# Kernel optimization log

Hardware: AMD Instinct MI355X
Metric: run time of the kernel (lower is better)

The kernel has to match this reference:

```python
import jax, jax.numpy as jnp
import numpy as np

DIM_MODEL = 1024
NUM_HEADS = 16
DIM_K = DIM_MODEL // NUM_HEADS
B, S = 4, 2048


def setup_inputs() -> dict:
    key = jax.random.key(0)
    ks = jax.random.split(key, 11)
    std = 1.0 / np.sqrt(DIM_MODEL)  # kaiming_normal fan_in, gain sqrt(2)/sqrt(fan_in); use simple scale
    kaiming = np.sqrt(2.0 / DIM_MODEL)
    return {
        "query": jax.random.normal(ks[0], (B, S, DIM_MODEL), dtype=jnp.float32),
        "key": jax.random.normal(ks[1], (B, S, DIM_MODEL), dtype=jnp.float32),
        "value": jax.random.normal(ks[2], (B, S, DIM_MODEL), dtype=jnp.float32),
        "W_q": jax.random.normal(ks[3], (DIM_MODEL, DIM_MODEL), dtype=jnp.float32) * kaiming,
        "b_q": jnp.zeros((DIM_MODEL,), dtype=jnp.float32),
        "W_k": jax.random.normal(ks[4], (DIM_MODEL, DIM_MODEL), dtype=jnp.float32) * kaiming,
        "b_k": jnp.zeros((DIM_MODEL,), dtype=jnp.float32),
        "W_v": jax.random.normal(ks[5], (DIM_MODEL, DIM_MODEL), dtype=jnp.float32) * kaiming,
        "b_v": jnp.zeros((DIM_MODEL,), dtype=jnp.float32),
        "W_o": jax.random.normal(ks[6], (DIM_MODEL, DIM_MODEL), dtype=jnp.float32) * kaiming,
        "b_o": jnp.zeros((DIM_MODEL,), dtype=jnp.float32),
    }


def _split_heads(x):
    b, s, _ = x.shape
    return x.reshape(b, s, NUM_HEADS, DIM_K).transpose(0, 2, 1, 3)  # [B,H,S,Dk]


def reference(query, key, value, W_q, b_q, W_k, b_k, W_v, b_v, W_o, b_o):
    # torch Linear: y = x @ W.T + b; dropout p=0.0 -> identity
    q = _split_heads(query @ W_q.T + b_q)
    k = _split_heads(key @ W_k.T + b_k)
    v = _split_heads(value @ W_v.T + b_v)
    scale = 1.0 / np.sqrt(DIM_K)
    scores = jnp.einsum("bhqd,bhkd->bhqk", q, k) * scale  # [B,H,S,S]
    probs = jax.nn.softmax(scores, axis=-1)
    attn = jnp.einsum("bhqk,bhkd->bhqd", probs, v)
    out = attn.transpose(0, 2, 1, 3).reshape(query.shape[0], query.shape[1], DIM_MODEL)
    return out @ W_o.T + b_o
```

## Files before the change

### kernel.cpp

```cpp
#include <hip/hip_runtime.h>
#include <stdint.h>

typedef __bf16 bf16x8 __attribute__((ext_vector_type(8)));
typedef __bf16 bf16x4 __attribute__((ext_vector_type(4)));
typedef float f32x4 __attribute__((ext_vector_type(4)));

static __device__ __forceinline__ unsigned short f2bf(float f) {
  unsigned u = __builtin_bit_cast(unsigned, f);
  u += 0x7fffu + ((u >> 16) & 1u);
  return (unsigned short)(u >> 16);
}

static __device__ __forceinline__ unsigned short bfu(float x) {
  __bf16 b = (__bf16)x;
  return __builtin_bit_cast(unsigned short, b);
}

#if __has_builtin(__builtin_amdgcn_exp2f)
#define EXP2(x) __builtin_amdgcn_exp2f(x)
#else
#define EXP2(x) __expf(0.69314718055994531f * (x))
#endif

static __device__ __forceinline__ void gload_lds16(const void* g, void* l) {
  __builtin_amdgcn_global_load_lds(
      (const __attribute__((address_space(1))) unsigned int*)(uintptr_t)g,
      (__attribute__((address_space(3))) unsigned int*)(uintptr_t)l, 16, 0, 0);
}

#define BIGU 2097152
#define WU   262144
__global__ __launch_bounds__(256) void cvt_all(const float* __restrict__ q,  const float* __restrict__ k,
                                               const float* __restrict__ v,  const float* __restrict__ wq,
                                               const float* __restrict__ wk, const float* __restrict__ wv,
                                               const float* __restrict__ wo, ushort4* __restrict__ dst) {
  int u = blockIdx.x * 256 + threadIdx.x;
  const float4* src;
  if (u < BIGU)            src = (const float4*)q + u;
  else if (u < 2 * BIGU)   src = (const float4*)k + (u - BIGU);
  else if (u < 3 * BIGU)   src = (const float4*)v + (u - 2 * BIGU);
  else {
    int r = u - 3 * BIGU;
    if (r < WU)            src = (const float4*)wq + r;
    else if (r < 2 * WU)   src = (const float4*)wk + (r - WU);
    else if (r < 3 * WU)   src = (const float4*)wv + (r - 2 * WU);
    else                   src = (const float4*)wo + (r - 3 * WU);
  }
  float4 f = *src;
  ushort4 o;
  o.x = f2bf(f.x); o.y = f2bf(f.y); o.z = f2bf(f.z); o.w = f2bf(f.w);
  dst[u] = o;
}

#define GM 8192
#define GN 1024
#define GK 1024

template <bool OUTF32>
__global__ __launch_bounds__(256) void gemm_bt(const unsigned short* __restrict__ A,
                                               const unsigned short* __restrict__ Bw,
                                               const float* __restrict__ bias,
                                               void* __restrict__ Cout) {
  __shared__ unsigned short As[128 * 64];
  __shared__ unsigned short Bs[128 * 64];
  const int tid = threadIdx.x;
  const int w = tid >> 6;
  const int lane = tid & 63;
  const int lq = lane & 15;
  const int g = lane >> 4;
  const int bm = blockIdx.y * 128;
  const int bn = blockIdx.x * 128;
  const int srow = lane >> 3;
  const int schunk = (lane & 7) ^ srow;
  const int wrow = (w >> 1) * 64;
  const int wcol = (w & 1) * 64;

  f32x4 acc[4][4] = {};

  for (int kt = 0; kt < GK / 64; ++kt) {
    __syncthreads();
#pragma unroll
    for (int j = 0; j < 4; ++j) {
      const int r0 = w * 32 + j * 8;
      const unsigned short* ag = A  + (size_t)(bm + r0 + srow) * GK + kt * 64 + schunk * 8;
      const unsigned short* bg = Bw + (size_t)(bn + r0 + srow) * GK + kt * 64 + schunk * 8;
      gload_lds16(ag, As + r0 * 64);
      gload_lds16(bg, Bs + r0 * 64);
    }
    __syncthreads();
#pragma unroll
    for (int kk = 0; kk < 2; ++kk) {
      bf16x8 af[4], bfv[4];
#pragma unroll
      for (int mt = 0; mt < 4; ++mt) {
        int m = wrow + mt * 16 + lq;
        af[mt] = *(const bf16x8*)&As[m * 64 + ((kk * 32 + g * 8) ^ ((m & 7) << 3))];
      }
#pragma unroll
      for (int nt = 0; nt < 4; ++nt) {
        int n = wcol + nt * 16 + lq;
        bfv[nt] = *(const bf16x8*)&Bs[n * 64 + ((kk * 32 + g * 8) ^ ((n & 7) << 3))];
      }
#pragma unroll
      for (int mt = 0; mt < 4; ++mt)
#pragma unroll
        for (int nt = 0; nt < 4; ++nt)
          acc[mt][nt] = __builtin_amdgcn_mfma_f32_16x16x32_bf16(af[mt], bfv[nt], acc[mt][nt], 0, 0, 0);
    }
  }

  float bvs[4];
#pragma unroll
  for (int nt = 0; nt < 4; ++nt) bvs[nt] = bias[bn + wcol + nt * 16 + lq];

#pragma unroll
  for (int mt = 0; mt < 4; ++mt) {
#pragma unroll
    for (int nt = 0; nt < 4; ++nt) {
#pragma unroll
      for (int r = 0; r < 4; ++r) {
        int m = bm + wrow + mt * 16 + g * 4 + r;
        int n = bn + wcol + nt * 16 + lq;
        float v = acc[mt][nt][r] + bvs[nt];
        if (OUTF32) ((float*)Cout)[(size_t)m * GN + n] = v;
        else        ((unsigned short*)Cout)[(size_t)m * GN + n] = f2bf(v);
      }
    }
  }
}

#define TRRD(dst, off) \
  asm volatile("ds_read_b64_tr_b16 %0, %1 offset:" off \
               : "=v"(dst) \
               : "v"((const __attribute__((address_space(3))) unsigned short*)(uintptr_t)vb))

__global__ __launch_bounds__(256, 3) void attn_fwd(const unsigned short* __restrict__ Qp,
                                                   const unsigned short* __restrict__ Kp,
                                                   const unsigned short* __restrict__ Vp,
                                                   unsigned short* __restrict__ Op) {
  __shared__ unsigned short Ks[2][4096];
  __shared__ unsigned short Vs[2][4096];
  __shared__ unsigned short Pl[8][1024];
  const int tid = threadIdx.x;
  const int w = tid >> 6;
  const int lane = tid & 63;
  const int lq = lane & 15;
  const int g = lane >> 4;
  const int qt = blockIdx.x;
  const int bh = blockIdx.y;
  const int b = bh >> 4;
  const int h = bh & 15;
  const size_t rowbase = (size_t)b * 2048;
  const int hcol = h * 64;

  const int c0 = w * 2, c1 = w * 2 + 1;
  const int srow = lane >> 3;
  const int schunk = (lane & 7) ^ srow;
  const int vkeyl = (lane >> 5) * 4 + ((lane >> 1) & 3);
  const int vd0   = ((lane >> 3) & 3) * 16 + (lane & 1) * 8;

  const unsigned short* kq = Kp + rowbase * 1024 + hcol;
  const unsigned short* vq = Vp + rowbase * 1024 + hcol;

  bf16x8 qf[2][2];
#pragma unroll
  for (int qh = 0; qh < 2; ++qh) {
    const int qrow = qt * 128 + w * 32 + qh * 16 + lq;
#pragma unroll
    for (int kk = 0; kk < 2; ++kk)
      qf[qh][kk] = *(const bf16x8*)&Qp[(rowbase + qrow) * 1024 + hcol + kk * 32 + g * 8];
  }

  const float ks2 = 0.125f * 1.44269504088896f;
  float m0 = -1e30f, m1 = -1e30f, l0 = 0.f, l1 = 0.f;
  f32x4 oa[2][4] = {};
  unsigned short* Pw0 = Pl[w * 2];
  unsigned short* Pw1 = Pl[w * 2 + 1];
  const int pxor = (lq & 7) << 3;
  const int kxor = pxor;

  {
    gload_lds16(kq + (size_t)(c0 * 8 + srow) * 1024 + schunk * 8, &Ks[0][c0 * 512]);
    gload_lds16(kq + (size_t)(c1 * 8 + srow) * 1024 + schunk * 8, &Ks[0][c1 * 512]);
    gload_lds16(vq + (size_t)(c0 * 8 + vkeyl) * 1024 + vd0, &Vs[0][c0 * 512]);
    gload_lds16(vq + (size_t)(c1 * 8 + vkeyl) * 1024 + vd0, &Vs[0][c1 * 512]);
  }
  __syncthreads();

  for (int j = 0; j < 32; ++j) {
    const int cur = j & 1;
    if (j < 31) {
      const size_t so = (size_t)(j + 1) * 64 * 1024;
      gload_lds16(kq + so + (size_t)(c0 * 8 + srow) * 1024 + schunk * 8, &Ks[cur ^ 1][c0 * 512]);
      gload_lds16(kq + so + (size_t)(c1 * 8 + srow) * 1024 + schunk * 8, &Ks[cur ^ 1][c1 * 512]);
      gload_lds16(vq + so + (size_t)(c0 * 8 + vkeyl) * 1024 + vd0, &Vs[cur ^ 1][c0 * 512]);
      gload_lds16(vq + so + (size_t)(c1 * 8 + vkeyl) * 1024 + vd0, &Vs[cur ^ 1][c1 * 512]);
    }

    f32x4 cc[2][4];
#pragma unroll
    for (int qh = 0; qh < 2; ++qh)
#pragma unroll
      for (int t = 0; t < 4; ++t) cc[qh][t] = (f32x4){0.f, 0.f, 0.f, 0.f};
#pragma unroll
    for (int t = 0; t < 4; ++t) {
      const int rb = (t * 16 + lq) * 64;
#pragma unroll
      for (int kk = 0; kk < 2; ++kk) {
        bf16x8 kf = *(const bf16x8*)&Ks[cur][rb + ((kk * 32 + g * 8) ^ kxor)];
        cc[0][t] = __builtin_amdgcn_mfma_f32_16x16x32_bf16(kf, qf[0][kk], cc[0][t], 0, 0, 0);
        cc[1][t] = __builtin_amdgcn_mfma_f32_16x16x32_bf16(kf, qf[1][kk], cc[1][t], 0, 0, 0);
      }
    }

    float t0 = cc[0][0][0], t1 = cc[1][0][0];
#pragma unroll
    for (int t = 0; t < 4; ++t)
#pragma unroll
      for (int r = 0; r < 4; ++r) {
        t0 = fmaxf(t0, cc[0][t][r]);
        t1 = fmaxf(t1, cc[1][t][r]);
      }
    t0 = fmaxf(t0, __shfl_xor(t0, 16)); t0 = fmaxf(t0, __shfl_xor(t0, 32));
    t1 = fmaxf(t1, __shfl_xor(t1, 16)); t1 = fmaxf(t1, __shfl_xor(t1, 32));

    const int defer = (t0 - m0 <= 64.f) && (t1 - m1 <= 64.f);
    if (!__all(defer)) {
      float n0 = fmaxf(m0, t0), n1 = fmaxf(m1, t1);
      float cr0 = EXP2(ks2 * (m0 - n0)), cr1 = EXP2(ks2 * (m1 - n1));
      l0 *= cr0; l1 *= cr1;
#pragma unroll
      for (int dt = 0; dt < 4; ++dt) { oa[0][dt] *= cr0; oa[1][dt] *= cr1; }
      m0 = n0; m1 = n1;
    }
    const float mk0 = m0 * ks2, mk1 = m1 * ks2;
    float ps0 = 0.f, ps1 = 0.f;
#pragma unroll
    for (int t = 0; t < 4; ++t) {
      float a0 = EXP2(__builtin_fmaf(cc[0][t][0], ks2, -mk0));
      float a1 = EXP2(__builtin_fmaf(cc[0][t][1], ks2, -mk0));
      float a2 = EXP2(__builtin_fmaf(cc[0][t][2], ks2, -mk0));
      float a3 = EXP2(__builtin_fmaf(cc[0][t][3], ks2, -mk0));
      ps0 += (a0 + a1) + (a2 + a3);
      ushort4 pk0; pk0.x = bfu(a0); pk0.y = bfu(a1); pk0.z = bfu(a2); pk0.w = bfu(a3);
      *(ushort4*)&Pw0[lq * 64 + ((t * 16 + g * 4) ^ pxor)] = pk0;
      float b0 = EXP2(__builtin_fmaf(cc[1][t][0], ks2, -mk1));
      float b1 = EXP2(__builtin_fmaf(cc[1][t][1], ks2, -mk1));
      float b2 = EXP2(__builtin_fmaf(cc[1][t][2], ks2, -mk1));
      float b3 = EXP2(__builtin_fmaf(cc[1][t][3], ks2, -mk1));
      ps1 += (b0 + b1) + (b2 + b3);
      ushort4 pk1; pk1.x = bfu(b0); pk1.y = bfu(b1); pk1.z = bfu(b2); pk1.w = bfu(b3);
      *(ushort4*)&Pw1[lq * 64 + ((t * 16 + g * 4) ^ pxor)] = pk1;
    }
    l0 += ps0; l1 += ps1;

    bf16x8 pf[2][2];
#pragma unroll
    for (int qh = 0; qh < 2; ++qh) {
      unsigned short* Pw = qh ? Pw1 : Pw0;
#pragma unroll
      for (int kk = 0; kk < 2; ++kk)
        pf[qh][kk] = *(const bf16x8*)&Pw[lq * 64 + ((kk * 32 + g * 8) ^ pxor)];
    }
    const unsigned short* vb =
        &Vs[cur][g * 512 + ((lane >> 2) & 3) * 16 + (lane & 3) * 4];
    bf16x4 T[16];
    TRRD(T[0],  "0");    TRRD(T[1],  "128");  TRRD(T[2],  "256");  TRRD(T[3],  "384");
    TRRD(T[4],  "512");  TRRD(T[5],  "640");  TRRD(T[6],  "768");  TRRD(T[7],  "896");
    TRRD(T[8],  "4096"); TRRD(T[9],  "4224"); TRRD(T[10], "4352"); TRRD(T[11], "4480");
    TRRD(T[12], "4608"); TRRD(T[13], "4736"); TRRD(T[14], "4864"); TRRD(T[15], "4992");
    asm volatile("s_waitcnt lgkmcnt(0)" ::: "memory");
    __builtin_amdgcn_sched_barrier(0);
#pragma unroll
    for (int kk = 0; kk < 2; ++kk) {
#pragma unroll
      for (int dt = 0; dt < 4; ++dt) {
        bf16x8 vf = __builtin_shufflevector(T[kk * 8 + dt], T[kk * 8 + 4 + dt],
                                            0, 1, 2, 3, 4, 5, 6, 7);
        oa[0][dt] = __builtin_amdgcn_mfma_f32_16x16x32_bf16(vf, pf[0][kk], oa[0][dt], 0, 0, 0);
        oa[1][dt] = __builtin_amdgcn_mfma_f32_16x16x32_bf16(vf, pf[1][kk], oa[1][dt], 0, 0, 0);
      }
    }
    __syncthreads();
  }

  l0 += __shfl_xor(l0, 16); l0 += __shfl_xor(l0, 32);
  l1 += __shfl_xor(l1, 16); l1 += __shfl_xor(l1, 32);
  float inv0 = 1.0f / l0, inv1 = 1.0f / l1;
#pragma unroll
  for (int qh = 0; qh < 2; ++qh) {
    const float inv = qh ? inv1 : inv0;
    const int qrow = qt * 128 + w * 32 + qh * 16 + lq;
#pragma unroll
    for (int dt = 0; dt < 4; ++dt) {
      ushort4 pk;
      pk.x = bfu(oa[qh][dt][0] * inv);
      pk.y = bfu(oa[qh][dt][1] * inv);
      pk.z = bfu(oa[qh][dt][2] * inv);
      pk.w = bfu(oa[qh][dt][3] * inv);
      *(ushort4*)&Op[(rowbase + qrow) * 1024 + hcol + dt * 16 + g * 4] = pk;
    }
  }
}

extern "C" void kernel_launch(void* const* d_in, const int* in_sizes, int n_in,
                              void* d_out, int out_size, void* d_ws, size_t ws_size,
                              hipStream_t stream) {
  const float* q  = (const float*)d_in[0];
  const float* k  = (const float*)d_in[1];
  const float* v  = (const float*)d_in[2];
  const float* Wq = (const float*)d_in[3];
  const float* bq = (const float*)d_in[4];
  const float* Wk = (const float*)d_in[5];
  const float* bk = (const float*)d_in[6];
  const float* Wv = (const float*)d_in[7];
  const float* bv = (const float*)d_in[8];
  const float* Wo = (const float*)d_in[9];
  const float* bo = (const float*)d_in[10];

  unsigned short* ws = (unsigned short*)d_ws;
  const size_t SZ  = (size_t)8192 * 1024;
  const size_t WSZ = (size_t)1024 * 1024;
  unsigned short* Xq  = ws;
  unsigned short* Xk  = Xq + SZ;
  unsigned short* Xv  = Xk + SZ;
  unsigned short* Wqb = Xv + SZ;
  unsigned short* Wkb = Wqb + WSZ;
  unsigned short* Wvb = Wkb + WSZ;
  unsigned short* Wob = Wvb + WSZ;
  unsigned short* Qp  = Wob + WSZ;
  unsigned short* Kp  = Qp + SZ;
  unsigned short* Vp  = Kp + SZ;
  unsigned short* At  = Xq;

  cvt_all<<<(3 * BIGU + 4 * WU) / 256, 256, 0, stream>>>(q, k, v, Wq, Wk, Wv, Wo, (ushort4*)ws);

  dim3 ggrid(GN / 128, GM / 128);
  gemm_bt<false><<<ggrid, 256, 0, stream>>>(Xq, Wqb, bq, Qp);
  gemm_bt<false><<<ggrid, 256, 0, stream>>>(Xk, Wkb, bk, Kp);
  gemm_bt<false><<<ggrid, 256, 0, stream>>>(Xv, Wvb, bv, Vp);

  attn_fwd<<<dim3(16, 64), 256, 0, stream>>>(Qp, Kp, Vp, At);

  gemm_bt<true><<<ggrid, 256, 0, stream>>>(At, Wob, bo, (float*)d_out);
}
```

Measured before the change: 358.2 us.

## Double-buffer GEMM LDS tiles and batch QKV projections into one launch

```diff
diff --git a/kernel.cpp b/kernel.cpp
--- a/kernel.cpp
+++ b/kernel.cpp
@@ -56,13 +56,20 @@
 #define GN 1024
 #define GK 1024
 
-template <bool OUTF32>
-__global__ __launch_bounds__(256) void gemm_bt(const unsigned short* __restrict__ A,
-                                               const unsigned short* __restrict__ Bw,
-                                               const float* __restrict__ bias,
-                                               void* __restrict__ Cout) {
-  __shared__ unsigned short As[128 * 64];
-  __shared__ unsigned short Bs[128 * 64];
+template <bool OUTF32, bool TRIPLE>
+__global__ __launch_bounds__(256, 2) void gemm_bt(const unsigned short* __restrict__ A0,
+                                                  const unsigned short* __restrict__ W0,
+                                                  const float* __restrict__ bias0,
+                                                  const float* __restrict__ bias1,
+                                                  const float* __restrict__ bias2,
+                                                  void* __restrict__ Cout) {
+  __shared__ unsigned short As[2][128 * 64];
+  __shared__ unsigned short Bs[2][128 * 64];
+  const int z = TRIPLE ? blockIdx.z : 0;
+  const unsigned short* A  = A0 + (size_t)z * ((size_t)GM * GK);
+  const unsigned short* Bw = W0 + (size_t)z * ((size_t)GN * GK);
+  const float* bias = TRIPLE ? (z == 0 ? bias0 : (z == 1 ? bias1 : bias2)) : bias0;
+
   const int tid = threadIdx.x;
   const int w = tid >> 6;
   const int lane = tid & 63;
@@ -77,29 +84,36 @@
 
   f32x4 acc[4][4] = {};
 
+#define STAGE(ktv, bufv)                                                                   \
+  do {                                                                                     \
+    _Pragma("unroll") for (int j = 0; j < 4; ++j) {                                        \
+      const int r0 = w * 32 + j * 8;                                                       \
+      gload_lds16(A  + (size_t)(bm + r0 + srow) * GK + (ktv) * 64 + schunk * 8,            \
+                  &As[bufv][r0 * 64]);                                                     \
+      gload_lds16(Bw + (size_t)(bn + r0 + srow) * GK + (ktv) * 64 + schunk * 8,            \
+                  &Bs[bufv][r0 * 64]);                                                     \
+    }                                                                                      \
+  } while (0)
+
+  STAGE(0, 0);
+  __syncthreads();
+
   for (int kt = 0; kt < GK / 64; ++kt) {
-    __syncthreads();
-#pragma unroll
-    for (int j = 0; j < 4; ++j) {
-      const int r0 = w * 32 + j * 8;
-      const unsigned short* ag = A  + (size_t)(bm + r0 + srow) * GK + kt * 64 + schunk * 8;
-      const unsigned short* bg = Bw + (size_t)(bn + r0 + srow) * GK + kt * 64 + schunk * 8;
-      gload_lds16(ag, As + r0 * 64);
-      gload_lds16(bg, Bs + r0 * 64);
-    }
-    __syncthreads();
+    const int cur = kt & 1;
+    if (kt < GK / 64 - 1) STAGE(kt + 1, cur ^ 1);
+
 #pragma unroll
     for (int kk = 0; kk < 2; ++kk) {
       bf16x8 af[4], bfv[4];
 #pragma unroll
       for (int mt = 0; mt < 4; ++mt) {
         int m = wrow + mt * 16 + lq;
-        af[mt] = *(const bf16x8*)&As[m * 64 + ((kk * 32 + g * 8) ^ ((m & 7) << 3))];
+        af[mt] = *(const bf16x8*)&As[cur][m * 64 + ((kk * 32 + g * 8) ^ ((m & 7) << 3))];
       }
 #pragma unroll
       for (int nt = 0; nt < 4; ++nt) {
         int n = wcol + nt * 16 + lq;
-        bfv[nt] = *(const bf16x8*)&Bs[n * 64 + ((kk * 32 + g * 8) ^ ((n & 7) << 3))];
+        bfv[nt] = *(const bf16x8*)&Bs[cur][n * 64 + ((kk * 32 + g * 8) ^ ((n & 7) << 3))];
       }
 #pragma unroll
       for (int mt = 0; mt < 4; ++mt)
@@ -107,7 +121,9 @@
         for (int nt = 0; nt < 4; ++nt)
           acc[mt][nt] = __builtin_amdgcn_mfma_f32_16x16x32_bf16(af[mt], bfv[nt], acc[mt][nt], 0, 0, 0);
     }
-  }
+    __syncthreads();
+  }
+#undef STAGE
 
   float bvs[4];
 #pragma unroll
@@ -123,7 +139,7 @@
         int n = bn + wcol + nt * 16 + lq;
         float v = acc[mt][nt][r] + bvs[nt];
         if (OUTF32) ((float*)Cout)[(size_t)m * GN + n] = v;
-        else        ((unsigned short*)Cout)[(size_t)m * GN + n] = f2bf(v);
+        else ((unsigned short*)Cout)[(size_t)z * ((size_t)GM * GN) + (size_t)m * GN + n] = f2bf(v);
       }
     }
   }
@@ -322,25 +338,18 @@
   const size_t SZ  = (size_t)8192 * 1024;
   const size_t WSZ = (size_t)1024 * 1024;
   unsigned short* Xq  = ws;
-  unsigned short* Xk  = Xq + SZ;
-  unsigned short* Xv  = Xk + SZ;
-  unsigned short* Wqb = Xv + SZ;
-  unsigned short* Wkb = Wqb + WSZ;
-  unsigned short* Wvb = Wkb + WSZ;
-  unsigned short* Wob = Wvb + WSZ;
-  unsigned short* Qp  = Wob + WSZ;
+  unsigned short* Wqb = Xq + 3 * SZ;
+  unsigned short* Qp  = Wqb + 4 * WSZ;
   unsigned short* Kp  = Qp + SZ;
   unsigned short* Vp  = Kp + SZ;
+  unsigned short* Wob = Wqb + 3 * WSZ;
   unsigned short* At  = Xq;
 
   cvt_all<<<(3 * BIGU + 4 * WU) / 256, 256, 0, stream>>>(q, k, v, Wq, Wk, Wv, Wo, (ushort4*)ws);
 
-  dim3 ggrid(GN / 128, GM / 128);
-  gemm_bt<false><<<ggrid, 256, 0, stream>>>(Xq, Wqb, bq, Qp);
-  gemm_bt<false><<<ggrid, 256, 0, stream>>>(Xk, Wkb, bk, Kp);
-  gemm_bt<false><<<ggrid, 256, 0, stream>>>(Xv, Wvb, bv, Vp);
+  gemm_bt<false, true><<<dim3(GN / 128, GM / 128, 3), 256, 0, stream>>>(Xq, Wqb, bq, bk, bv, Qp);
 
   attn_fwd<<<dim3(16, 64), 256, 0, stream>>>(Qp, Kp, Vp, At);
 
-  gemm_bt<true><<<ggrid, 256, 0, stream>>>(At, Wob, bo, (float*)d_out);
-}
+  gemm_bt<true, false><<<dim3(GN / 128, GM / 128, 1), 256, 0, stream>>>(At, Wob, bo, bo, bo, (float*)d_out);
+}
```

Result: no change. 353.8 us (-1.2%).
